# Kernel tuning notes

Hardware: AMD Instinct MI355X
Metric: run time of the kernel (lower is better)

Reference implementation:

```python
import jax, jax.numpy as jnp
import numpy as np

K = 3          # kernel_size == n_qubits
STRIDES = 1
OUT_FILTERS = 64


def _apply_rx(state, theta):
    """Apply RX(theta) on the qubit whose axis was moved to -via flip axis- caller supplies axis."""
    raise NotImplementedError  # replaced below (kept minimal); see _rx


def _rx(state, theta, axis):
    # state: (N, 2, 2, 2) complex64; theta: (N,) or scalar
    half = jnp.asarray(theta) * 0.5
    c = jnp.cos(half)
    s = jnp.sin(half)
    # append trailing singleton dims so (N,) broadcasts over the qubit axes
    c = jnp.reshape(c, c.shape + (1,) * (state.ndim - c.ndim))
    s = jnp.reshape(s, s.shape + (1,) * (state.ndim - s.ndim))
    flipped = jnp.flip(state, axis)  # Pauli-X on that qubit
    return c * state - 1j * s * flipped


def _cnot(state, c_ax, t_ax):
    s0 = jax.lax.index_in_dim(state, 0, c_ax, keepdims=True)
    s1 = jnp.flip(jax.lax.index_in_dim(state, 1, c_ax, keepdims=True), t_ax)
    return jnp.concatenate([s0, s1], axis=c_ax)


def _vqc_expval_z0(angles, weights):
    """AngleEmbedding(RX) + BasicEntanglerLayers(RX + CNOT ring), expval PauliZ(0).
    angles: (N, K) float32, weights: (L, K) float32 -> (N,) float32."""
    N = angles.shape[0]
    state = jnp.zeros((N,) + (2,) * K, jnp.complex64)
    state = state.at[(slice(None),) + (0,) * K].set(1.0)
    # angle embedding: RX(x_q) on qubit q
    for q in range(K):
        state = _rx(state, angles[:, q], axis=1 + q)
    # entangler layers
    if K == 2:
        pairs = [(0, 1)]
    elif K > 2:
        pairs = [(i, (i + 1) % K) for i in range(K)]
    else:
        pairs = []
    for l in range(weights.shape[0]):
        for q in range(K):
            state = _rx(state, weights[l, q], axis=1 + q)
        for cq, tq in pairs:
            state = _cnot(state, 1 + cq, 1 + tq)
    probs = state.real ** 2 + state.imag ** 2            # (N, 2, 2, 2)
    p = probs.reshape(N, 2, -1).sum(-1)                  # marginal on qubit 0
    return p[:, 0] - p[:, 1]


def setup_inputs() -> dict:
    key = jax.random.key(0)
    kx, kw = jax.random.split(key)
    x = jax.random.normal(kx, (32, 256, 256), dtype=jnp.float32)
    # TorchLayer weights for BasicEntanglerLayers: (n_qlayers, n_qubits)
    weights = jax.random.uniform(kw, (1, K), dtype=jnp.float32) * (2.0 * np.pi)
    return {"x": x, "weights": weights}


def reference(x, weights):
    B, W, C = x.shape
    k, s = K, STRIDES
    out_width = (C - (k - 1) - 1) // s + 1               # from the original size formula
    m_idx = np.arange(0, W - k, s)                       # matches range(0, W - k, s)
    M = len(m_idx)
    # windows over dim1: (B, M, k, C)
    win = x[:, m_idx[:, None] + np.arange(k)[None, :], :]
    # torch .reshape(-1, k) on a (k, C) slice is a ROW-MAJOR reshape to (C, k)
    rows = win.reshape(B, M, C, k)
    ev = _vqc_expval_z0(rows.reshape(-1, k), weights).reshape(B, M, C)
    vals = ev.sum(-1)                                     # (B, M): sum of per-row expvals
    out = jnp.zeros((B, out_width, OUT_FILTERS), x.dtype)
    # same scalar written for every output filter j
    out = out.at[:, m_idx, :].set(jnp.broadcast_to(vals[:, :, None], (B, M, OUT_FILTERS)))
    return out
```

## Files before the change

### kernel.cpp

```cpp
#include <hip/hip_runtime.h>
#include <math.h>


constexpr int Bn = 32;
constexpr int Wn = 256;
constexpr int Cn = 256;
constexpr int Mn = 253;
constexpr int OW = 254;
constexpr int OF = 64;

__global__ __launch_bounds__(256)
void qconv1d_kernel(const float* __restrict__ x,
                    const float* __restrict__ wt,
                    float* __restrict__ out) {
    const int bid = blockIdx.x;
    const int b   = bid / OW;
    const int m   = bid - b * OW;
    const int t   = threadIdx.x;

    float* orow = out + ((size_t)b * OW + m) * OF;

    if (m >= Mn) {
        if (t < OF) orow[t] = 0.0f;
        return;
    }

    const float w1 = wt[1];
    const float w2 = wt[2];

    const float* wf = x + ((size_t)b * Wn + m) * Cn;
    const float a1 = wf[3 * t + 1];
    const float a2 = wf[3 * t + 2];
    float v = cosf(a1 + w1) * cosf(a2 + w2);

    #pragma unroll
    for (int off = 32; off > 0; off >>= 1)
        v += __shfl_down(v, off, 64);

    __shared__ float parts[4];
    if ((t & 63) == 0) parts[t >> 6] = v;
    __syncthreads();

    if (t < OF) {
        const float total = parts[0] + parts[1] + parts[2] + parts[3];
        orow[t] = total;
    }
}

extern "C" void kernel_launch(void* const* d_in, const int* in_sizes, int n_in,
                              void* d_out, int out_size, void* d_ws, size_t ws_size,
                              hipStream_t stream) {
    const float* x  = (const float*)d_in[0];
    const float* wt = (const float*)d_in[1];
    float* out = (float*)d_out;

    qconv1d_kernel<<<dim3(Bn * OW), dim3(256), 0, stream>>>(x, wt, out);
}
```

Measured before the change: 11.73 us.

## Process four output rows per block with shared-memory tiling and fast cosine

Each block now covers four consecutive window positions instead of one. It loads the six overlapping input rows into shared memory with float4 loads, and each wavefront computes one output row by reducing with xor shuffles. This removes the cross-wave shared reduction, reuses overlapping rows, and cuts the block count. It also swaps cosf for __cosf, which lowers accuracy for large arguments.

```diff
diff --git a/kernel.cpp b/kernel.cpp
--- a/kernel.cpp
+++ b/kernel.cpp
@@ -8,43 +8,59 @@
 constexpr int Mn = 253;
 constexpr int OW = 254;
 constexpr int OF = 64;
+constexpr int MPB = 4;
 
 __global__ __launch_bounds__(256)
 void qconv1d_kernel(const float* __restrict__ x,
                     const float* __restrict__ wt,
                     float* __restrict__ out) {
+    __shared__ float tile[6 * Cn];
+
     const int bid = blockIdx.x;
-    const int b   = bid / OW;
-    const int m   = bid - b * OW;
+    const int b   = bid >> 6;
+    const int g   = bid & 63;
+    const int m0  = g * MPB;
     const int t   = threadIdx.x;
 
+    const float* xb = x + (size_t)b * Wn * Cn;
+    #pragma unroll
+    for (int i = t; i < 384; i += 256) {
+        int row  = m0 + (i >> 6);
+        int rowc = row < Wn ? row : Wn - 1;
+        reinterpret_cast<float4*>(tile)[i] =
+            reinterpret_cast<const float4*>(xb + (size_t)rowc * Cn)[i & 63];
+    }
+    __syncthreads();
+
+    const int w    = t >> 6;
+    const int lane = t & 63;
+    const int m    = m0 + w;
+    if (m >= OW) return;
+
     float* orow = out + ((size_t)b * OW + m) * OF;
-
     if (m >= Mn) {
-        if (t < OF) orow[t] = 0.0f;
+        orow[lane] = 0.0f;
         return;
     }
 
     const float w1 = wt[1];
     const float w2 = wt[2];
+    const float* wrow = tile + w * Cn;
 
-    const float* wf = x + ((size_t)b * Wn + m) * Cn;
-    const float a1 = wf[3 * t + 1];
-    const float a2 = wf[3 * t + 2];
-    float v = cosf(a1 + w1) * cosf(a2 + w2);
+    float acc = 0.0f;
+    #pragma unroll
+    for (int i = 0; i < 4; ++i) {
+        const int c = i * 64 + lane;
+        const float a1 = wrow[3 * c + 1];
+        const float a2 = wrow[3 * c + 2];
+        acc += __cosf(a1 + w1) * __cosf(a2 + w2);
+    }
 
     #pragma unroll
     for (int off = 32; off > 0; off >>= 1)
-        v += __shfl_down(v, off, 64);
+        acc += __shfl_xor(acc, off, 64);
 
-    __shared__ float parts[4];
-    if ((t & 63) == 0) parts[t >> 6] = v;
-    __syncthreads();
-
-    if (t < OF) {
-        const float total = parts[0] + parts[1] + parts[2] + parts[3];
-        orow[t] = total;
-    }
+    orow[lane] = acc;
 }
 
 extern "C" void kernel_launch(void* const* d_in, const int* in_sizes, int n_in,
@@ -54,5 +70,5 @@
     const float* wt = (const float*)d_in[1];
     float* out = (float*)d_out;
 
-    qconv1d_kernel<<<dim3(Bn * OW), dim3(256), 0, stream>>>(x, wt, out);
+    qconv1d_kernel<<<dim3(Bn * 64), dim3(256), 0, stream>>>(x, wt, out);
 }
```

Result: faster. 10.15 us (-13.5%).
